# Kernel tuning notes

Hardware: AMD Instinct MI355X
Metric: run time of the kernel (lower is better)

The kernel has to match this reference:

```python
import jax, jax.numpy as jnp
import numpy as np

B = 131072
INPUT_SIZE = 128
HIDDEN_SIZE = 128


def setup_inputs() -> dict:
    key = jax.random.key(0)
    ks = jax.random.split(key, 11)
    stdv = 1.0 / (HIDDEN_SIZE ** 0.5)

    def unif(k, shape):
        return jax.random.uniform(k, shape, dtype=jnp.float32, minval=-stdv, maxval=stdv)

    return {
        "x_t": jax.random.normal(ks[0], (B, INPUT_SIZE), dtype=jnp.float32),
        "h_prev": jax.random.normal(ks[1], (B, HIDDEN_SIZE), dtype=jnp.float32),
        "Wz": unif(ks[2], (INPUT_SIZE, HIDDEN_SIZE)),
        "Uz": unif(ks[3], (HIDDEN_SIZE, HIDDEN_SIZE)),
        "bz": unif(ks[4], (HIDDEN_SIZE,)),
        "Wr": unif(ks[5], (INPUT_SIZE, HIDDEN_SIZE)),
        "Ur": unif(ks[6], (HIDDEN_SIZE, HIDDEN_SIZE)),
        "br": unif(ks[7], (HIDDEN_SIZE,)),
        "Wh": unif(ks[8], (INPUT_SIZE, HIDDEN_SIZE)),
        "Uh": unif(ks[9], (HIDDEN_SIZE, HIDDEN_SIZE)),
        "bh": unif(ks[10], (HIDDEN_SIZE,)),
    }


def reference(x_t, h_prev, Wz, Uz, bz, Wr, Ur, br, Wh, Uh, bh):
    # Fuse the three input-side and two hidden-side GEMMs by concatenating weights.
    W = jnp.concatenate([Wz, Wr, Wh], axis=1)        # [I, 3H]
    U = jnp.concatenate([Uz, Ur], axis=1)            # [H, 2H]
    xw = x_t @ W                                     # [B, 3H]
    hu = h_prev @ U                                  # [B, 2H]
    H = bz.shape[0]
    z_t = jax.nn.sigmoid(xw[:, :H] + hu[:, :H] + bz)
    r_t = jax.nn.sigmoid(xw[:, H:2 * H] + hu[:, H:] + br)
    h_cand = jnp.tanh(xw[:, 2 * H:] + (r_t * h_prev) @ Uh + bh)
    h_t = (1.0 - z_t) * h_prev + z_t * h_cand
    return h_t
```

## Files before the change

### kernel.cpp

```cpp
#include <hip/hip_runtime.h>
#include <hip/hip_bf16.h>

typedef __attribute__((ext_vector_type(8))) short bf16x8;
typedef __attribute__((ext_vector_type(4))) float f32x4;

#define GRU_B 131072
#define BM 32

static __device__ __forceinline__ ushort f2bf(float f) {
  union { float f; unsigned u; } v; v.f = f;
  unsigned r = v.u + 0x7FFFu + ((v.u >> 16) & 1u);
  return (ushort)(r >> 16);
}
static __device__ __forceinline__ float bf2f(ushort u) {
  union { unsigned u; float f; } v; v.u = ((unsigned)u) << 16;
  return v.f;
}
static __device__ __forceinline__ unsigned pk2(float a, float b) {
  float2 t; t.x = a; t.y = b;
  __hip_bfloat162 r = __float22bfloat162_rn(t);
  union { __hip_bfloat162 b; unsigned u; } cv; cv.b = r;
  return cv.u;
}
static __device__ __forceinline__ float fsig(float x) {
  return __builtin_amdgcn_rcpf(1.0f + __expf(-x));
}
static __device__ __forceinline__ float ftanh(float x) {
  return 1.0f - 2.0f * __builtin_amdgcn_rcpf(1.0f + __expf(2.0f * x));
}
static __device__ __forceinline__ f32x4 splat4(float s) {
  f32x4 v = {s, s, s, s}; return v;
}

__global__ void wtrans_kernel(const float* __restrict__ wz, const float* __restrict__ uz,
                              const float* __restrict__ wr, const float* __restrict__ ur,
                              const float* __restrict__ wh, const float* __restrict__ uh,
                              ushort* __restrict__ outw) {
  int f = blockIdx.x * 256 + threadIdx.x;
  int mat = f >> 14;
  int rem = f & 16383;
  int chunk = rem >> 9;
  int lane = (rem >> 3) & 63;
  int e = rem & 7;
  int cb = chunk >> 2, k0b = chunk & 3;
  int n = cb * 16 + (lane & 15);
  int k = k0b * 32 + (lane >> 4) * 8 + e;
  const float* src = (mat == 0) ? wz : (mat == 1) ? uz : (mat == 2) ? wr
                   : (mat == 3) ? ur : (mat == 4) ? wh : uh;
  outw[f] = f2bf(src[k * 128 + n]);
}

#define MFMA __builtin_amdgcn_mfma_f32_16x16x32_bf16

__global__ __launch_bounds__(256, 4) void gru_kernel(
    const float* __restrict__ x, const float* __restrict__ hprev,
    const ushort* __restrict__ wt,
    const float* __restrict__ bz, const float* __restrict__ br,
    const float* __restrict__ bh, float* __restrict__ out) {
  __shared__ __align__(16) char smem[24576];
  ushort* xs  = (ushort*)smem;
  ushort* hs  = (ushort*)(smem + 8192);
  ushort* rhs = (ushort*)(smem + 16384);

  const int tid = threadIdx.x;
  const int lane = tid & 63;
  const int wid = tid >> 6;
  const int l15 = lane & 15;
  const int q = lane >> 4;
  const long row0 = (long)blockIdx.x * BM;
  const int n0 = wid * 32;

  float brv0 = br[n0 + l15], brv1 = br[n0 + 16 + l15];
  float bzv0 = bz[n0 + l15], bzv1 = bz[n0 + 16 + l15];
  float bhv0 = bh[n0 + l15], bhv1 = bh[n0 + 16 + l15];

  const ushort* wlane = wt + (lane << 3);
  auto wfrag = [&](int mat, int nc, int kb) -> const bf16x8* {
    return (const bf16x8*)(wlane + (((((mat << 3) + (wid << 1) + nc) << 2) + kb) << 9));
  };

  bf16x8 rB[4][4];
#pragma unroll
  for (int kb = 0; kb < 4; ++kb) {
    rB[kb][0] = *wfrag(2, 0, kb); rB[kb][1] = *wfrag(2, 1, kb);
    rB[kb][2] = *wfrag(3, 0, kb); rB[kb][3] = *wfrag(3, 1, kb);
  }

  {
    const float4* xg = (const float4*)(x + row0 * 128);
    const float4* hg = (const float4*)(hprev + row0 * 128);
#pragma unroll
    for (int i = 0; i < 4; ++i) {
      int idx = i * 256 + tid;
      int r = idx >> 5;
      int cb = (idx & 31) << 3;
      int bo = (r * 256 + cb) ^ ((r & 7) << 4);
      float4 xv = xg[idx];
      float4 hv = hg[idx];
      uint2 xp, hp;
      xp.x = pk2(xv.x, xv.y); xp.y = pk2(xv.z, xv.w);
      hp.x = pk2(hv.x, hv.y); hp.y = pk2(hv.z, hv.w);
      *(uint2*)(smem + bo) = xp;
      *(uint2*)(smem + 8192 + bo) = hp;
    }
  }
  __syncthreads();

  auto ldsA = [&](const ushort* base, int mr, int k0) -> bf16x8 {
    int row = mr * 16 + l15;
    int bo = (row * 256 + (k0 + q * 8) * 2) ^ ((row & 7) << 4);
    return *(const bf16x8*)((const char*)base + bo);
  };

  f32x4 accr[2][2];
#pragma unroll
  for (int mr = 0; mr < 2; ++mr) {
    accr[mr][0] = splat4(brv0); accr[mr][1] = splat4(brv1);
  }
#pragma unroll
  for (int kb = 0; kb < 4; ++kb) {
#pragma unroll
    for (int mr = 0; mr < 2; ++mr) {
      bf16x8 ax = ldsA(xs, mr, kb * 32);
      bf16x8 ah = ldsA(hs, mr, kb * 32);
      accr[mr][0] = MFMA(ax, rB[kb][0], accr[mr][0], 0, 0, 0);
      accr[mr][1] = MFMA(ax, rB[kb][1], accr[mr][1], 0, 0, 0);
      accr[mr][0] = MFMA(ah, rB[kb][2], accr[mr][0], 0, 0, 0);
      accr[mr][1] = MFMA(ah, rB[kb][3], accr[mr][1], 0, 0, 0);
    }
  }

  bf16x8 mB[2][8];
  mB[0][0] = *wfrag(0, 0, 0); mB[0][1] = *wfrag(0, 1, 0);
  mB[0][2] = *wfrag(1, 0, 0); mB[0][3] = *wfrag(1, 1, 0);
  mB[0][4] = *wfrag(4, 0, 0); mB[0][5] = *wfrag(4, 1, 0);
  mB[0][6] = *wfrag(5, 0, 0); mB[0][7] = *wfrag(5, 1, 0);

#pragma unroll
  for (int mr = 0; mr < 2; ++mr)
#pragma unroll
    for (int nc = 0; nc < 2; ++nc)
#pragma unroll
      for (int j = 0; j < 4; ++j) {
        int row = mr * 16 + q * 4 + j;
        int col = n0 + nc * 16 + l15;
        float rv = fsig(accr[mr][nc][j]);
        int bo = (row * 256 + col * 2) ^ ((row & 7) << 4);
        float hp = bf2f(*(const ushort*)((const char*)hs + bo));
        *(ushort*)((char*)rhs + bo) = f2bf(rv * hp);
      }

  __syncthreads();

  f32x4 accz[2][2], acch[2][2];
#pragma unroll
  for (int mr = 0; mr < 2; ++mr) {
    accz[mr][0] = splat4(bzv0); accz[mr][1] = splat4(bzv1);
    acch[mr][0] = splat4(bhv0); acch[mr][1] = splat4(bhv1);
  }
#pragma unroll
  for (int kb = 0; kb < 4; ++kb) {
    const int cur = kb & 1, nxt = cur ^ 1;
    if (kb < 3) {
      mB[nxt][0] = *wfrag(0, 0, kb + 1); mB[nxt][1] = *wfrag(0, 1, kb + 1);
      mB[nxt][2] = *wfrag(1, 0, kb + 1); mB[nxt][3] = *wfrag(1, 1, kb + 1);
      mB[nxt][4] = *wfrag(4, 0, kb + 1); mB[nxt][5] = *wfrag(4, 1, kb + 1);
      mB[nxt][6] = *wfrag(5, 0, kb + 1); mB[nxt][7] = *wfrag(5, 1, kb + 1);
    }
#pragma unroll
    for (int mr = 0; mr < 2; ++mr) {
      bf16x8 ax = ldsA(xs, mr, kb * 32);
      bf16x8 ah = ldsA(hs, mr, kb * 32);
      bf16x8 ar = ldsA(rhs, mr, kb * 32);
      accz[mr][0] = MFMA(ax, mB[cur][0], accz[mr][0], 0, 0, 0);
      accz[mr][1] = MFMA(ax, mB[cur][1], accz[mr][1], 0, 0, 0);
      accz[mr][0] = MFMA(ah, mB[cur][2], accz[mr][0], 0, 0, 0);
      accz[mr][1] = MFMA(ah, mB[cur][3], accz[mr][1], 0, 0, 0);
      acch[mr][0] = MFMA(ax, mB[cur][4], acch[mr][0], 0, 0, 0);
      acch[mr][1] = MFMA(ax, mB[cur][5], acch[mr][1], 0, 0, 0);
      acch[mr][0] = MFMA(ar, mB[cur][6], acch[mr][0], 0, 0, 0);
      acch[mr][1] = MFMA(ar, mB[cur][7], acch[mr][1], 0, 0, 0);
    }
  }

#pragma unroll
  for (int mr = 0; mr < 2; ++mr)
#pragma unroll
    for (int nc = 0; nc < 2; ++nc)
#pragma unroll
      for (int j = 0; j < 4; ++j) {
        int row = mr * 16 + q * 4 + j;
        int col = n0 + nc * 16 + l15;
        float hc = ftanh(acch[mr][nc][j]);
        float zv = fsig(accz[mr][nc][j]);
        int bo = (row * 256 + col * 2) ^ ((row & 7) << 4);
        float hp = bf2f(*(const ushort*)((const char*)hs + bo));
        acch[mr][nc][j] = hp + zv * (hc - hp);
      }

  __syncthreads();

  {
    float* ot = (float*)smem;
#pragma unroll
    for (int mr = 0; mr < 2; ++mr)
#pragma unroll
      for (int nc = 0; nc < 2; ++nc)
#pragma unroll
        for (int j = 0; j < 4; ++j) {
          int row = mr * 16 + q * 4 + j;
          int col = n0 + nc * 16 + l15;
          int bo = (row * 512 + col * 4) ^ ((row & 7) << 4);
          *(float*)((char*)ot + bo) = acch[mr][nc][j];
        }
  }

  __syncthreads();

  {
#pragma unroll
    for (int i = 0; i < 4; ++i) {
      int idx = i * 256 + tid;
      int row = idx >> 5;
      int c4 = idx & 31;
      int bo = (row * 512 + c4 * 16) ^ ((row & 7) << 4);
      float4 v = *(const float4*)(smem + bo);
      *(float4*)(out + (row0 + row) * 128 + c4 * 4) = v;
    }
  }
}

extern "C" void kernel_launch(void* const* d_in, const int* in_sizes, int n_in,
                              void* d_out, int out_size, void* d_ws, size_t ws_size,
                              hipStream_t stream) {
  const float* x  = (const float*)d_in[0];
  const float* h  = (const float*)d_in[1];
  const float* Wz = (const float*)d_in[2];
  const float* Uz = (const float*)d_in[3];
  const float* bz = (const float*)d_in[4];
  const float* Wr = (const float*)d_in[5];
  const float* Ur = (const float*)d_in[6];
  const float* br = (const float*)d_in[7];
  const float* Wh = (const float*)d_in[8];
  const float* Uh = (const float*)d_in[9];
  const float* bh = (const float*)d_in[10];
  ushort* wt = (ushort*)d_ws;

  hipLaunchKernelGGL(wtrans_kernel, dim3(384), dim3(256), 0, stream,
                     Wz, Uz, Wr, Ur, Wh, Uh, wt);
  hipLaunchKernelGGL(gru_kernel, dim3(GRU_B / BM), dim3(256), 0, stream,
                     x, h, wt, bz, br, bh, (float*)d_out);
}
```

Baseline: 60.24 us.

## Use 8 waves per block with 16-column slices and single fused MFMA pass

Doubles the block to 512 threads so each of 8 waves owns a 16-column output slice instead of 32. All of the r, z and h-input GEMMs are computed in one pass over K. The Uh GEMM runs afterwards on r*h written in place over the x tile, which drops the separate rhs buffer and shrinks shared memory from 24 KB to 16 KB. This aims to raise occupancy and cut register pressure and redundant LDS reads. The cost is more waves reading the same A tiles and one extra barrier.

Result: slower. 82.58 us (+37.1%).

```diff
diff --git a/kernel.cpp b/kernel.cpp
--- a/kernel.cpp
+++ b/kernel.cpp
@@ -52,15 +52,14 @@
 
 #define MFMA __builtin_amdgcn_mfma_f32_16x16x32_bf16
 
-__global__ __launch_bounds__(256, 4) void gru_kernel(
+__global__ __launch_bounds__(512, 8) void gru_kernel(
     const float* __restrict__ x, const float* __restrict__ hprev,
     const ushort* __restrict__ wt,
     const float* __restrict__ bz, const float* __restrict__ br,
     const float* __restrict__ bh, float* __restrict__ out) {
-  __shared__ __align__(16) char smem[24576];
-  ushort* xs  = (ushort*)smem;
-  ushort* hs  = (ushort*)(smem + 8192);
-  ushort* rhs = (ushort*)(smem + 16384);
+  __shared__ __align__(16) char smem[16384];
+  ushort* xs = (ushort*)smem;
+  ushort* hs = (ushort*)(smem + 8192);
 
   const int tid = threadIdx.x;
   const int lane = tid & 63;
@@ -68,33 +67,26 @@
   const int l15 = lane & 15;
   const int q = lane >> 4;
   const long row0 = (long)blockIdx.x * BM;
-  const int n0 = wid * 32;
-
-  float brv0 = br[n0 + l15], brv1 = br[n0 + 16 + l15];
-  float bzv0 = bz[n0 + l15], bzv1 = bz[n0 + 16 + l15];
-  float bhv0 = bh[n0 + l15], bhv1 = bh[n0 + 16 + l15];
+  const int n0 = wid * 16;
+
+  float brv = br[n0 + l15];
+  float bzv = bz[n0 + l15];
+  float bhv = bh[n0 + l15];
 
   const ushort* wlane = wt + (lane << 3);
-  auto wfrag = [&](int mat, int nc, int kb) -> const bf16x8* {
-    return (const bf16x8*)(wlane + (((((mat << 3) + (wid << 1) + nc) << 2) + kb) << 9));
+  auto wfrag = [&](int mat, int kb) -> const bf16x8* {
+    return (const bf16x8*)(wlane + ((((mat << 3) + wid) << 2) + kb) * 512);
   };
-
-  bf16x8 rB[4][4];
-#pragma unroll
-  for (int kb = 0; kb < 4; ++kb) {
-    rB[kb][0] = *wfrag(2, 0, kb); rB[kb][1] = *wfrag(2, 1, kb);
-    rB[kb][2] = *wfrag(3, 0, kb); rB[kb][3] = *wfrag(3, 1, kb);
-  }
 
   {
     const float4* xg = (const float4*)(x + row0 * 128);
     const float4* hg = (const float4*)(hprev + row0 * 128);
 #pragma unroll
-    for (int i = 0; i < 4; ++i) {
-      int idx = i * 256 + tid;
+    for (int i = 0; i < 2; ++i) {
+      int idx = i * 512 + tid;
       int r = idx >> 5;
-      int cb = (idx & 31) << 3;
-      int bo = (r * 256 + cb) ^ ((r & 7) << 4);
+      int cbyte = (idx & 31) << 3;
+      int bo = (r * 256 + cbyte) ^ ((r & 7) << 4);
       float4 xv = xg[idx];
       float4 hv = hg[idx];
       uint2 xp, hp;
@@ -112,115 +104,90 @@
     return *(const bf16x8*)((const char*)base + bo);
   };
 
-  f32x4 accr[2][2];
+  f32x4 accr[2], accz[2], acch[2];
 #pragma unroll
   for (int mr = 0; mr < 2; ++mr) {
-    accr[mr][0] = splat4(brv0); accr[mr][1] = splat4(brv1);
+    accr[mr] = splat4(brv); accz[mr] = splat4(bzv); acch[mr] = splat4(bhv);
   }
 #pragma unroll
   for (int kb = 0; kb < 4; ++kb) {
+    bf16x8 bWz = *wfrag(0, kb);
+    bf16x8 bUz = *wfrag(1, kb);
+    bf16x8 bWr = *wfrag(2, kb);
+    bf16x8 bUr = *wfrag(3, kb);
+    bf16x8 bWh = *wfrag(4, kb);
 #pragma unroll
     for (int mr = 0; mr < 2; ++mr) {
       bf16x8 ax = ldsA(xs, mr, kb * 32);
       bf16x8 ah = ldsA(hs, mr, kb * 32);
-      accr[mr][0] = MFMA(ax, rB[kb][0], accr[mr][0], 0, 0, 0);
-      accr[mr][1] = MFMA(ax, rB[kb][1], accr[mr][1], 0, 0, 0);
-      accr[mr][0] = MFMA(ah, rB[kb][2], accr[mr][0], 0, 0, 0);
-      accr[mr][1] = MFMA(ah, rB[kb][3], accr[mr][1], 0, 0, 0);
-    }
-  }
-
-  bf16x8 mB[2][8];
-  mB[0][0] = *wfrag(0, 0, 0); mB[0][1] = *wfrag(0, 1, 0);
-  mB[0][2] = *wfrag(1, 0, 0); mB[0][3] = *wfrag(1, 1, 0);
-  mB[0][4] = *wfrag(4, 0, 0); mB[0][5] = *wfrag(4, 1, 0);
-  mB[0][6] = *wfrag(5, 0, 0); mB[0][7] = *wfrag(5, 1, 0);
+      accr[mr] = MFMA(ax, bWr, accr[mr], 0, 0, 0);
+      accr[mr] = MFMA(ah, bUr, accr[mr], 0, 0, 0);
+      accz[mr] = MFMA(ax, bWz, accz[mr], 0, 0, 0);
+      accz[mr] = MFMA(ah, bUz, accz[mr], 0, 0, 0);
+      acch[mr] = MFMA(ax, bWh, acch[mr], 0, 0, 0);
+    }
+  }
+
+  bf16x8 bUh0 = *wfrag(5, 0), bUh1 = *wfrag(5, 1);
+  bf16x8 bUh2 = *wfrag(5, 2), bUh3 = *wfrag(5, 3);
+
+  __syncthreads();
 
 #pragma unroll
   for (int mr = 0; mr < 2; ++mr)
 #pragma unroll
-    for (int nc = 0; nc < 2; ++nc)
+    for (int j = 0; j < 4; ++j) {
+      int row = mr * 16 + q * 4 + j;
+      int col = n0 + l15;
+      float rv = fsig(accr[mr][j]);
+      int bo = (row * 256 + col * 2) ^ ((row & 7) << 4);
+      float hp = bf2f(*(const ushort*)((const char*)hs + bo));
+      *(ushort*)((char*)xs + bo) = f2bf(rv * hp);
+    }
+
+  __syncthreads();
+
+#pragma unroll
+  for (int mr = 0; mr < 2; ++mr) {
+    acch[mr] = MFMA(ldsA(xs, mr, 0),  bUh0, acch[mr], 0, 0, 0);
+    acch[mr] = MFMA(ldsA(xs, mr, 32), bUh1, acch[mr], 0, 0, 0);
+    acch[mr] = MFMA(ldsA(xs, mr, 64), bUh2, acch[mr], 0, 0, 0);
+    acch[mr] = MFMA(ldsA(xs, mr, 96), bUh3, acch[mr], 0, 0, 0);
+  }
+
+#pragma unroll
+  for (int mr = 0; mr < 2; ++mr)
+#pragma unroll
+    for (int j = 0; j < 4; ++j) {
+      int row = mr * 16 + q * 4 + j;
+      int col = n0 + l15;
+      float hc = ftanh(acch[mr][j]);
+      float zv = fsig(accz[mr][j]);
+      int bo = (row * 256 + col * 2) ^ ((row & 7) << 4);
+      float hp = bf2f(*(const ushort*)((const char*)hs + bo));
+      acch[mr][j] = hp + zv * (hc - hp);
+    }
+
+  __syncthreads();
+
+  {
+#pragma unroll
+    for (int mr = 0; mr < 2; ++mr)
 #pragma unroll
       for (int j = 0; j < 4; ++j) {
         int row = mr * 16 + q * 4 + j;
-        int col = n0 + nc * 16 + l15;
-        float rv = fsig(accr[mr][nc][j]);
-        int bo = (row * 256 + col * 2) ^ ((row & 7) << 4);
-        float hp = bf2f(*(const ushort*)((const char*)hs + bo));
-        *(ushort*)((char*)rhs + bo) = f2bf(rv * hp);
+        int col = n0 + l15;
+        int bo = (row * 512 + col * 4) ^ ((row & 7) << 4);
+        *(float*)(smem + bo) = acch[mr][j];
       }
-
-  __syncthreads();
-
-  f32x4 accz[2][2], acch[2][2];
-#pragma unroll
-  for (int mr = 0; mr < 2; ++mr) {
-    accz[mr][0] = splat4(bzv0); accz[mr][1] = splat4(bzv1);
-    acch[mr][0] = splat4(bhv0); acch[mr][1] = splat4(bhv1);
-  }
-#pragma unroll
-  for (int kb = 0; kb < 4; ++kb) {
-    const int cur = kb & 1, nxt = cur ^ 1;
-    if (kb < 3) {
-      mB[nxt][0] = *wfrag(0, 0, kb + 1); mB[nxt][1] = *wfrag(0, 1, kb + 1);
-      mB[nxt][2] = *wfrag(1, 0, kb + 1); mB[nxt][3] = *wfrag(1, 1, kb + 1);
-      mB[nxt][4] = *wfrag(4, 0, kb + 1); mB[nxt][5] = *wfrag(4, 1, kb + 1);
-      mB[nxt][6] = *wfrag(5, 0, kb + 1); mB[nxt][7] = *wfrag(5, 1, kb + 1);
-    }
-#pragma unroll
-    for (int mr = 0; mr < 2; ++mr) {
-      bf16x8 ax = ldsA(xs, mr, kb * 32);
-      bf16x8 ah = ldsA(hs, mr, kb * 32);
-      bf16x8 ar = ldsA(rhs, mr, kb * 32);
-      accz[mr][0] = MFMA(ax, mB[cur][0], accz[mr][0], 0, 0, 0);
-      accz[mr][1] = MFMA(ax, mB[cur][1], accz[mr][1], 0, 0, 0);
-      accz[mr][0] = MFMA(ah, mB[cur][2], accz[mr][0], 0, 0, 0);
-      accz[mr][1] = MFMA(ah, mB[cur][3], accz[mr][1], 0, 0, 0);
-      acch[mr][0] = MFMA(ax, mB[cur][4], acch[mr][0], 0, 0, 0);
-      acch[mr][1] = MFMA(ax, mB[cur][5], acch[mr][1], 0, 0, 0);
-      acch[mr][0] = MFMA(ar, mB[cur][6], acch[mr][0], 0, 0, 0);
-      acch[mr][1] = MFMA(ar, mB[cur][7], acch[mr][1], 0, 0, 0);
-    }
-  }
-
-#pragma unroll
-  for (int mr = 0; mr < 2; ++mr)
-#pragma unroll
-    for (int nc = 0; nc < 2; ++nc)
-#pragma unroll
-      for (int j = 0; j < 4; ++j) {
-        int row = mr * 16 + q * 4 + j;
-        int col = n0 + nc * 16 + l15;
-        float hc = ftanh(acch[mr][nc][j]);
-        float zv = fsig(accz[mr][nc][j]);
-        int bo = (row * 256 + col * 2) ^ ((row & 7) << 4);
-        float hp = bf2f(*(const ushort*)((const char*)hs + bo));
-        acch[mr][nc][j] = hp + zv * (hc - hp);
-      }
+  }
 
   __syncthreads();
 
   {
-    float* ot = (float*)smem;
-#pragma unroll
-    for (int mr = 0; mr < 2; ++mr)
-#pragma unroll
-      for (int nc = 0; nc < 2; ++nc)
-#pragma unroll
-        for (int j = 0; j < 4; ++j) {
-          int row = mr * 16 + q * 4 + j;
-          int col = n0 + nc * 16 + l15;
-          int bo = (row * 512 + col * 4) ^ ((row & 7) << 4);
-          *(float*)((char*)ot + bo) = acch[mr][nc][j];
-        }
-  }
-
-  __syncthreads();
-
-  {
-#pragma unroll
-    for (int i = 0; i < 4; ++i) {
-      int idx = i * 256 + tid;
+#pragma unroll
+    for (int i = 0; i < 2; ++i) {
+      int idx = i * 512 + tid;
       int row = idx >> 5;
       int c4 = idx & 31;
       int bo = (row * 512 + c4 * 16) ^ ((row & 7) << 4);
@@ -248,6 +215,6 @@
 
   hipLaunchKernelGGL(wtrans_kernel, dim3(384), dim3(256), 0, stream,
                      Wz, Uz, Wr, Ur, Wh, Uh, wt);
-  hipLaunchKernelGGL(gru_kernel, dim3(GRU_B / BM), dim3(256), 0, stream,
+  hipLaunchKernelGGL(gru_kernel, dim3(GRU_B / BM), dim3(512), 0, stream,
                      x, h, wt, bz, br, bh, (float*)d_out);
 }
```

## Double GRU row tile to 64 and load weight fragments per k-block

Applied to the files above, without the earlier changes.

Raises the rows per block from 32 to 64, doubling shared memory to 48KB and the accumulator count per wave. Each weight fragment loaded from global memory now feeds four MFMA row tiles instead of two, which halves weight traffic per output row and halves the block count. The earlier preload of all reset-gate weights and the double-buffered prefetch are replaced by plain per-k-block loads. The larger shared-memory and register footprint may lower occupancy, and the weight loads are no longer prefetched ahead of the MFMAs.

After: 87.23 us. +44.8%, slower.

```diff
diff --git a/kernel.cpp b/kernel.cpp
--- a/kernel.cpp
+++ b/kernel.cpp
@@ -5,7 +5,7 @@
 typedef __attribute__((ext_vector_type(4))) float f32x4;
 
 #define GRU_B 131072
-#define BM 32
+#define BM 64
 
 static __device__ __forceinline__ ushort f2bf(float f) {
   union { float f; unsigned u; } v; v.f = f;
@@ -57,10 +57,10 @@
     const ushort* __restrict__ wt,
     const float* __restrict__ bz, const float* __restrict__ br,
     const float* __restrict__ bh, float* __restrict__ out) {
-  __shared__ __align__(16) char smem[24576];
+  __shared__ __align__(16) char smem[49152];
   ushort* xs  = (ushort*)smem;
-  ushort* hs  = (ushort*)(smem + 8192);
-  ushort* rhs = (ushort*)(smem + 16384);
+  ushort* hs  = (ushort*)(smem + 16384);
+  ushort* rhs = (ushort*)(smem + 32768);
 
   const int tid = threadIdx.x;
   const int lane = tid & 63;
@@ -79,29 +79,22 @@
     return (const bf16x8*)(wlane + (((((mat << 3) + (wid << 1) + nc) << 2) + kb) << 9));
   };
 
-  bf16x8 rB[4][4];
-#pragma unroll
-  for (int kb = 0; kb < 4; ++kb) {
-    rB[kb][0] = *wfrag(2, 0, kb); rB[kb][1] = *wfrag(2, 1, kb);
-    rB[kb][2] = *wfrag(3, 0, kb); rB[kb][3] = *wfrag(3, 1, kb);
-  }
-
   {
     const float4* xg = (const float4*)(x + row0 * 128);
     const float4* hg = (const float4*)(hprev + row0 * 128);
 #pragma unroll
-    for (int i = 0; i < 4; ++i) {
+    for (int i = 0; i < 8; ++i) {
       int idx = i * 256 + tid;
       int r = idx >> 5;
-      int cb = (idx & 31) << 3;
-      int bo = (r * 256 + cb) ^ ((r & 7) << 4);
+      int cbyte = (idx & 31) << 3;
+      int bo = (r * 256 + cbyte) ^ ((r & 7) << 4);
       float4 xv = xg[idx];
       float4 hv = hg[idx];
       uint2 xp, hp;
       xp.x = pk2(xv.x, xv.y); xp.y = pk2(xv.z, xv.w);
       hp.x = pk2(hv.x, hv.y); hp.y = pk2(hv.z, hv.w);
       *(uint2*)(smem + bo) = xp;
-      *(uint2*)(smem + 8192 + bo) = hp;
+      *(uint2*)(smem + 16384 + bo) = hp;
     }
   }
   __syncthreads();
@@ -112,32 +105,28 @@
     return *(const bf16x8*)((const char*)base + bo);
   };
 
-  f32x4 accr[2][2];
-#pragma unroll
-  for (int mr = 0; mr < 2; ++mr) {
+  f32x4 accr[4][2];
+#pragma unroll
+  for (int mr = 0; mr < 4; ++mr) {
     accr[mr][0] = splat4(brv0); accr[mr][1] = splat4(brv1);
   }
 #pragma unroll
   for (int kb = 0; kb < 4; ++kb) {
-#pragma unroll
-    for (int mr = 0; mr < 2; ++mr) {
+    bf16x8 b0 = *wfrag(2, 0, kb), b1 = *wfrag(2, 1, kb);
+    bf16x8 c0 = *wfrag(3, 0, kb), c1 = *wfrag(3, 1, kb);
+#pragma unroll
+    for (int mr = 0; mr < 4; ++mr) {
       bf16x8 ax = ldsA(xs, mr, kb * 32);
       bf16x8 ah = ldsA(hs, mr, kb * 32);
-      accr[mr][0] = MFMA(ax, rB[kb][0], accr[mr][0], 0, 0, 0);
-      accr[mr][1] = MFMA(ax, rB[kb][1], accr[mr][1], 0, 0, 0);
-      accr[mr][0] = MFMA(ah, rB[kb][2], accr[mr][0], 0, 0, 0);
-      accr[mr][1] = MFMA(ah, rB[kb][3], accr[mr][1], 0, 0, 0);
-    }
-  }
-
-  bf16x8 mB[2][8];
-  mB[0][0] = *wfrag(0, 0, 0); mB[0][1] = *wfrag(0, 1, 0);
-  mB[0][2] = *wfrag(1, 0, 0); mB[0][3] = *wfrag(1, 1, 0);
-  mB[0][4] = *wfrag(4, 0, 0); mB[0][5] = *wfrag(4, 1, 0);
-  mB[0][6] = *wfrag(5, 0, 0); mB[0][7] = *wfrag(5, 1, 0);
-
-#pragma unroll
-  for (int mr = 0; mr < 2; ++mr)
+      accr[mr][0] = MFMA(ax, b0, accr[mr][0], 0, 0, 0);
+      accr[mr][1] = MFMA(ax, b1, accr[mr][1], 0, 0, 0);
+      accr[mr][0] = MFMA(ah, c0, accr[mr][0], 0, 0, 0);
+      accr[mr][1] = MFMA(ah, c1, accr[mr][1], 0, 0, 0);
+    }
+  }
+
+#pragma unroll
+  for (int mr = 0; mr < 4; ++mr)
 #pragma unroll
     for (int nc = 0; nc < 2; ++nc)
 #pragma unroll
@@ -152,39 +141,36 @@
 
   __syncthreads();
 
-  f32x4 accz[2][2], acch[2][2];
-#pragma unroll
-  for (int mr = 0; mr < 2; ++mr) {
+  f32x4 accz[4][2], acch[4][2];
+#pragma unroll
+  for (int mr = 0; mr < 4; ++mr) {
     accz[mr][0] = splat4(bzv0); accz[mr][1] = splat4(bzv1);
     acch[mr][0] = splat4(bhv0); acch[mr][1] = splat4(bhv1);
   }
 #pragma unroll
   for (int kb = 0; kb < 4; ++kb) {
-    const int cur = kb & 1, nxt = cur ^ 1;
-    if (kb < 3) {
-      mB[nxt][0] = *wfrag(0, 0, kb + 1); mB[nxt][1] = *wfrag(0, 1, kb + 1);
-      mB[nxt][2] = *wfrag(1, 0, kb + 1); mB[nxt][3] = *wfrag(1, 1, kb + 1);
-      mB[nxt][4] = *wfrag(4, 0, kb + 1); mB[nxt][5] = *wfrag(4, 1, kb + 1);
-      mB[nxt][6] = *wfrag(5, 0, kb + 1); mB[nxt][7] = *wfrag(5, 1, kb + 1);
-    }
-#pragma unroll
-    for (int mr = 0; mr < 2; ++mr) {
+    bf16x8 z0 = *wfrag(0, 0, kb), z1 = *wfrag(0, 1, kb);
+    bf16x8 u0 = *wfrag(1, 0, kb), u1 = *wfrag(1, 1, kb);
+    bf16x8 w0 = *wfrag(4, 0, kb), w1 = *wfrag(4, 1, kb);
+    bf16x8 v0 = *wfrag(5, 0, kb), v1 = *wfrag(5, 1, kb);
+#pragma unroll
+    for (int mr = 0; mr < 4; ++mr) {
       bf16x8 ax = ldsA(xs, mr, kb * 32);
       bf16x8 ah = ldsA(hs, mr, kb * 32);
       bf16x8 ar = ldsA(rhs, mr, kb * 32);
-      accz[mr][0] = MFMA(ax, mB[cur][0], accz[mr][0], 0, 0, 0);
-      accz[mr][1] = MFMA(ax, mB[cur][1], accz[mr][1], 0, 0, 0);
-      accz[mr][0] = MFMA(ah, mB[cur][2], accz[mr][0], 0, 0, 0);
-      accz[mr][1] = MFMA(ah, mB[cur][3], accz[mr][1], 0, 0, 0);
-      acch[mr][0] = MFMA(ax, mB[cur][4], acch[mr][0], 0, 0, 0);
-      acch[mr][1] = MFMA(ax, mB[cur][5], acch[mr][1], 0, 0, 0);
-      acch[mr][0] = MFMA(ar, mB[cur][6], acch[mr][0], 0, 0, 0);
-      acch[mr][1] = MFMA(ar, mB[cur][7], acch[mr][1], 0, 0, 0);
-    }
-  }
-
-#pragma unroll
-  for (int mr = 0; mr < 2; ++mr)
+      accz[mr][0] = MFMA(ax, z0, accz[mr][0], 0, 0, 0);
+      accz[mr][1] = MFMA(ax, z1, accz[mr][1], 0, 0, 0);
+      accz[mr][0] = MFMA(ah, u0, accz[mr][0], 0, 0, 0);
+      accz[mr][1] = MFMA(ah, u1, accz[mr][1], 0, 0, 0);
+      acch[mr][0] = MFMA(ax, w0, acch[mr][0], 0, 0, 0);
+      acch[mr][1] = MFMA(ax, w1, acch[mr][1], 0, 0, 0);
+      acch[mr][0] = MFMA(ar, v0, acch[mr][0], 0, 0, 0);
+      acch[mr][1] = MFMA(ar, v1, acch[mr][1], 0, 0, 0);
+    }
+  }
+
+#pragma unroll
+  for (int mr = 0; mr < 4; ++mr)
 #pragma unroll
     for (int nc = 0; nc < 2; ++nc)
 #pragma unroll
@@ -201,9 +187,8 @@
   __syncthreads();
 
   {
-    float* ot = (float*)smem;
-#pragma unroll
-    for (int mr = 0; mr < 2; ++mr)
+#pragma unroll
+    for (int mr = 0; mr < 4; ++mr)
 #pragma unroll
       for (int nc = 0; nc < 2; ++nc)
 #pragma unroll
@@ -211,7 +196,7 @@
           int row = mr * 16 + q * 4 + j;
           int col = n0 + nc * 16 + l15;
           int bo = (row * 512 + col * 4) ^ ((row & 7) << 4);
-          *(float*)((char*)ot + bo) = acch[mr][nc][j];
+          *(float*)(smem + bo) = acch[mr][nc][j];
         }
   }
 
@@ -219,7 +204,7 @@
 
   {
 #pragma unroll
-    for (int i = 0; i < 4; ++i) {
+    for (int i = 0; i < 8; ++i) {
       int idx = i * 256 + tid;
       int row = idx >> 5;
       int c4 = idx & 31;
```
